# Kernel tuning notes

Hardware: AMD Instinct MI355X
Metric: run time of the kernel (lower is better)

The kernel has to match this reference:

```python
import jax, jax.numpy as jnp
import numpy as np

B, D, H, NSTEPS = 4096, 512, 2048, 16


def setup_inputs() -> dict:
    key = jax.random.key(0)
    k1, k2, k3, k4 = jax.random.split(key, 4)
    s_x = 1.0 / np.sqrt(D)
    s_h = 1.0 / np.sqrt(H)
    return {
        "z_in": jax.random.normal(k1, (B, D), dtype=jnp.float32),
        "Wx": jax.random.normal(k2, (D, H), dtype=jnp.float32) * s_x,
        "Wh": jax.random.normal(k3, (H, H), dtype=jnp.float32) * s_h,
        "bh": jnp.zeros((H,), dtype=jnp.float32),
        "Wout": jax.random.normal(k4, (H, D), dtype=jnp.float32) * s_h,
        "bout": jnp.zeros((D,), dtype=jnp.float32),
        "n_steps": NSTEPS,
    }


def reference(z_in, Wx, Wh, bh, Wout, bout, n_steps):
    # Input projection is identical every step (same z_in fed each iteration).
    xproj = z_in @ Wx + bh  # [B, H]
    h0 = jnp.zeros((z_in.shape[0], Wh.shape[0]), dtype=z_in.dtype)

    def step(h, _):
        h_new = jnp.tanh(xproj + h @ Wh)          # Elman RNN cell, hidden retained
        out = h_new @ Wout + bout                  # MLP head hidden -> latent
        return h_new, out

    _, outs = jax.lax.scan(step, h0, None, length=n_steps)  # [n_steps, B, D]
    return jnp.transpose(outs, (1, 0, 2))  # torch.stack(outs, 1) -> [B, n_steps, D]
```

## Files before the change

kernel.cpp:

```cpp
#include <hip/hip_runtime.h>
#include <hip/hip_bf16.h>
#include <stdint.h>

#define B_ 4096
#define D_ 512
#define H_ 2048
#define NS_ 16

typedef __bf16 bf16x8 __attribute__((ext_vector_type(8)));
typedef float f32x4 __attribute__((ext_vector_type(4)));
typedef short short4v __attribute__((ext_vector_type(4)));
typedef __attribute__((address_space(3))) const bf16x8* lds_frag_p;

__device__ __forceinline__ short f2bf(float f) {
  union { float f; uint32_t u; } c; c.f = f;
  uint32_t u = c.u;
  return (short)((u + 0x7fffu + ((u >> 16) & 1u)) >> 16);
}

__device__ __forceinline__ float tanh_fast(float x) {
  float e = __expf(2.0f * x);
  return 1.0f - 2.0f / (e + 1.0f);
}

__device__ __forceinline__ void gload16(const void* g, void* l) {
  __builtin_amdgcn_global_load_lds((const __attribute__((address_space(1))) void*)g,
                                   (__attribute__((address_space(3))) void*)l,
                                   16, 0, 0);
}

__global__ __launch_bounds__(256, 3) void gemm128_fusedB(
    const short* __restrict__ A, const short* __restrict__ Wfrag, int K,
    const float* __restrict__ xproj, const float* __restrict__ bias,
    float* __restrict__ outf, short* __restrict__ outh, int tout)
{
  __shared__ short lds[4 * 4096];
  const int tid = threadIdx.x, lane = tid & 63, wid = tid >> 6;
  const int wm = wid >> 1, wn = wid & 1;
  const int NT = K >> 5;

  const int g = ((int)blockIdx.x & 7) * 80 + ((int)blockIdx.x >> 3);
  const int tm = g & 31, tn = g >> 5;
  const int row0 = tm * 128, col0 = tn * 128;

  const int r0 = wid * 16 + (lane >> 2), r1 = r0 + 64;
  const int sl = lane & 3;
  const short* gA0 = A + (size_t)(row0 + r0) * K + ((sl ^ ((r0 >> 1) & 3)) << 3);
  const short* gA1 = A + (size_t)(row0 + r1) * K + ((sl ^ ((r1 >> 1) & 3)) << 3);
  const int dls = r0 * 32 + sl * 8;

  auto stageA = [&](int kt) {
    const int d = (kt & 3) * 4096 + dls;
    const size_t ko = (size_t)kt * 32;
    gload16(gA0 + ko, &lds[d]);
    gload16(gA1 + ko, &lds[d + 2048]);
  };

  const int rr = lane & 15, s4 = lane >> 4;
  int offA[4];
#pragma unroll
  for (int m = 0; m < 4; ++m) {
    int r = wm * 64 + m * 16 + rr;
    offA[m] = r * 32 + ((s4 ^ ((r >> 1) & 3)) << 3);
  }

  const short* bf = Wfrag + (size_t)(tn * 8 + wn * 4) * NT * 512 + lane * 8;

  f32x4 acc[4][4];
#pragma unroll
  for (int m = 0; m < 4; ++m)
#pragma unroll
    for (int n = 0; n < 4; ++n)
      acc[m][n] = (f32x4){0.f, 0.f, 0.f, 0.f};

  bf16x8 aX[4], bX[4], aY[4], bY[4];

  stageA(0); stageA(1); stageA(2);
#pragma unroll
  for (int n = 0; n < 4; ++n) bX[n] = *(const bf16x8*)(bf + (size_t)n * NT * 512);
  asm volatile("s_waitcnt vmcnt(0)" ::: "memory");
  __builtin_amdgcn_s_barrier();
#pragma unroll
  for (int m = 0; m < 4; ++m) aX[m] = *(lds_frag_p)&lds[offA[m]];

  auto iter = [&](int kt, bf16x8 (&ac)[4], bf16x8 (&bc)[4],
                  bf16x8 (&an)[4], bf16x8 (&bn)[4]) {
    const int kn = kt + 1;
    if (kn < NT) {
#pragma unroll
      for (int n = 0; n < 4; ++n)
        bn[n] = *(const bf16x8*)(bf + ((size_t)n * NT + kn) * 512);
    }
    if (kt + 3 < NT) stageA(kt + 3);
    if (kn < NT) {
      const int bb = (kn & 3) * 4096;
#pragma unroll
      for (int m = 0; m < 4; ++m) an[m] = *(lds_frag_p)&lds[bb + offA[m]];
    }
#pragma unroll
    for (int m = 0; m < 4; ++m)
#pragma unroll
      for (int n = 0; n < 4; ++n)
        acc[m][n] = __builtin_amdgcn_mfma_f32_16x16x32_bf16(ac[m], bc[n], acc[m][n], 0, 0, 0);
    if (kt + 3 < NT) {
      asm volatile("s_waitcnt vmcnt(2)" ::: "memory");
    } else {
      asm volatile("s_waitcnt vmcnt(0)" ::: "memory");
    }
    asm volatile("s_waitcnt lgkmcnt(0)" ::: "memory");
    if (kt < NT - 1) __builtin_amdgcn_s_barrier();
  };

  for (int kt = 0; kt < NT; kt += 2) {
    iter(kt,     aX, bX, aY, bY);
    iter(kt + 1, aY, bY, aX, bX);
  }

  const int rb = row0 + wm * 64 + ((lane >> 4) << 2);
  const int cb = col0 + wn * 64 + (lane & 15);
#pragma unroll
  for (int m = 0; m < 4; ++m) {
#pragma unroll
    for (int n = 0; n < 4; ++n) {
      const int col = cb + n * 16;
#pragma unroll
      for (int r = 0; r < 4; ++r) {
        const int row = rb + m * 16 + r;
        float v = acc[m][n][r];
        if (col < H_) {
          float x = xproj[(size_t)row * H_ + col];
          outh[(size_t)row * H_ + col] = f2bf(tanh_fast(x + v));
        } else {
          int oc = col - H_;
          outf[(size_t)row * (NS_ * D_) + tout * D_ + oc] = v + bias[oc];
        }
      }
    }
  }
}

__global__ void wfrag_build(const float* __restrict__ Wh, const float* __restrict__ Wout,
                            short* __restrict__ Wfrag) {
  const int k = blockIdx.y;
  const int col = blockIdx.x * 256 + threadIdx.x;
  float v = (col < H_) ? Wh[(size_t)k * H_ + col]
                       : Wout[(size_t)k * D_ + (col - H_)];
  Wfrag[((size_t)(col >> 4) * 64 + (k >> 5)) * 512 +
        ((k >> 3) & 3) * 128 + (col & 15) * 8 + (k & 7)] = f2bf(v);
}

template<int BM, int BN, int EPI>
__global__ __launch_bounds__(256, 2) void gemm_bt(
    const short* __restrict__ A, const short* __restrict__ Bt, int K,
    const float* __restrict__ xproj, const float* __restrict__ bias,
    float* __restrict__ outf, short* __restrict__ outh, int ldN, int tout)
{
  constexpr int WM = BM / 2, WN = BN / 2;
  constexpr int RM = WM / 16, RN = WN / 16;
  __shared__ short lds[2][(BM + BN) * 32];
  const int tid = threadIdx.x, lane = tid & 63, wid = tid >> 6;
  const int wm = wid >> 1, wn = wid & 1;
  const int row0 = blockIdx.y * BM, col0 = blockIdx.x * BN;
  const short* Ag = A + (size_t)row0 * K;
  const short* Bg = Bt + (size_t)col0 * K;

  f32x4 acc[RM][RN];
#pragma unroll
  for (int m = 0; m < RM; ++m)
#pragma unroll
    for (int n = 0; n < RN; ++n)
      acc[m][n] = (f32x4){0.f, 0.f, 0.f, 0.f};

  const int nt = K >> 5;

  auto stage = [&](int kt, int buf) {
    const short* ga = Ag + (kt << 5);
#pragma unroll
    for (int i = 0; i < BM * 4; i += 256) {
      int slot = i + tid;
      gload16(ga + (size_t)(slot >> 2) * K + ((slot & 3) << 3), &lds[buf][slot * 8]);
    }
    const short* gb = Bg + (kt << 5);
#pragma unroll
    for (int i = 0; i < BN * 4; i += 256) {
      int slot = i + tid;
      gload16(gb + (size_t)(slot >> 2) * K + ((slot & 3) << 3),
              &lds[buf][BM * 32 + slot * 8]);
    }
  };

  stage(0, 0);
  __syncthreads();
  int cur = 0;
  const int kq = (lane >> 4) << 3;
  const int rr = lane & 15;
  for (int kt = 0; kt < nt; ++kt) {
    if (kt + 1 < nt) stage(kt + 1, cur ^ 1);
    const short* la = &lds[cur][(wm * WM) * 32];
    const short* lb = &lds[cur][BM * 32 + (wn * WN) * 32];
    bf16x8 a[RM], b[RN];
#pragma unroll
    for (int m = 0; m < RM; ++m)
      a[m] = *(const bf16x8*)(la + (m * 16 + rr) * 32 + kq);
#pragma unroll
    for (int n = 0; n < RN; ++n)
      b[n] = *(const bf16x8*)(lb + (n * 16 + rr) * 32 + kq);
#pragma unroll
    for (int m = 0; m < RM; ++m)
#pragma unroll
      for (int n = 0; n < RN; ++n)
        acc[m][n] = __builtin_amdgcn_mfma_f32_16x16x32_bf16(a[m], b[n], acc[m][n], 0, 0, 0);
    __syncthreads();
    cur ^= 1;
  }

  const int rb = row0 + wm * WM + ((lane >> 4) << 2);
  const int cb = col0 + wn * WN + (lane & 15);
#pragma unroll
  for (int m = 0; m < RM; ++m) {
#pragma unroll
    for (int n = 0; n < RN; ++n) {
      const int col = cb + n * 16;
#pragma unroll
      for (int r = 0; r < 4; ++r) {
        const int row = rb + m * 16 + r;
        float v = acc[m][n][r];
        if (EPI == 0) {
          outf[(size_t)row * ldN + col] = v + bias[col];
        } else {
          outf[(size_t)row * (NS_ * D_) + tout * D_ + col] = v + bias[col];
        }
      }
    }
  }
}

__global__ void transpose_cvt(const float* __restrict__ in, short* __restrict__ out,
                              int R, int C) {
  __shared__ float tile[32][33];
  const int tx = threadIdx.x & 31, ty = threadIdx.x >> 5;
  const int c0 = blockIdx.x * 32, r0 = blockIdx.y * 32;
#pragma unroll
  for (int i = 0; i < 32; i += 8)
    tile[ty + i][tx] = in[(size_t)(r0 + ty + i) * C + c0 + tx];
  __syncthreads();
#pragma unroll
  for (int i = 0; i < 32; i += 8)
    out[(size_t)(c0 + ty + i) * R + r0 + tx] = f2bf(tile[tx][ty + i]);
}

__global__ void cvt_bf16_k(const float4* __restrict__ in, short4v* __restrict__ out, int n4) {
  int i = blockIdx.x * 256 + threadIdx.x;
  if (i >= n4) return;
  float4 v = in[i];
  short4v o;
  o[0] = f2bf(v.x); o[1] = f2bf(v.y); o[2] = f2bf(v.z); o[3] = f2bf(v.w);
  out[i] = o;
}

__global__ void tanh_h0_k(const float4* __restrict__ xp, short4v* __restrict__ h, int n4) {
  int i = blockIdx.x * 256 + threadIdx.x;
  if (i >= n4) return;
  float4 v = xp[i];
  short4v o;
  o[0] = f2bf(tanh_fast(v.x)); o[1] = f2bf(tanh_fast(v.y));
  o[2] = f2bf(tanh_fast(v.z)); o[3] = f2bf(tanh_fast(v.w));
  h[i] = o;
}

extern "C" void kernel_launch(void* const* d_in, const int* in_sizes, int n_in,
                              void* d_out, int out_size, void* d_ws, size_t ws_size,
                              hipStream_t stream) {
  const float* z    = (const float*)d_in[0];
  const float* Wx   = (const float*)d_in[1];
  const float* Wh   = (const float*)d_in[2];
  const float* bh   = (const float*)d_in[3];
  const float* Wout = (const float*)d_in[4];
  const float* bout = (const float*)d_in[5];
  float* out = (float*)d_out;

  short* zb    = (short*)d_ws;
  short* WxT   = zb + (size_t)B_ * D_;
  short* WoutT = WxT + (size_t)H_ * D_;
  short* Wfrag = WoutT + (size_t)D_ * H_;
  short* h0    = Wfrag + (size_t)(H_ + D_) * H_;
  short* h1    = h0 + (size_t)B_ * H_;
  float* xproj = (float*)(h1 + (size_t)B_ * H_);

  cvt_bf16_k<<<(B_ * D_ / 4 + 255) / 256, 256, 0, stream>>>((const float4*)z, (short4v*)zb, B_ * D_ / 4);
  transpose_cvt<<<dim3(H_ / 32, D_ / 32), 256, 0, stream>>>(Wx, WxT, D_, H_);
  transpose_cvt<<<dim3(D_ / 32, H_ / 32), 256, 0, stream>>>(Wout, WoutT, H_, D_);
  wfrag_build<<<dim3((H_ + D_) / 256, H_), 256, 0, stream>>>(Wh, Wout, Wfrag);

  gemm_bt<128, 128, 0><<<dim3(H_ / 128, B_ / 128), 256, 0, stream>>>(
      zb, WxT, D_, nullptr, bh, xproj, nullptr, H_, 0);
  tanh_h0_k<<<(B_ * H_ / 4 + 255) / 256, 256, 0, stream>>>((const float4*)xproj, (short4v*)h0, B_ * H_ / 4);

  short* hb[2] = {h0, h1};
  for (int t = 1; t <= 15; ++t) {
    const short* hp = hb[(t - 1) & 1];
    short* hn = hb[t & 1];
    gemm128_fusedB<<<640, 256, 0, stream>>>(
        hp, Wfrag, H_, xproj, bout, out, hn, t - 1);
  }
  gemm_bt<128, 64, 2><<<dim3(D_ / 64, B_ / 128), 256, 0, stream>>>(
      hb[1], WoutT, H_, nullptr, bout, out, nullptr, 0, 15);
}
```

Baseline: 1.261 ms.

## Replace LDS-staged 128x128 fused GEMM with single-wave 64x64 direct-load kernel

The recurrent step GEMM switches from a 4-wave 128x128 tile that staged A through a multi-buffered LDS ring to a single-wave 64x64 tile that loads A fragments straight from global memory into registers. This removes the LDS traffic, async-copy waits and block barriers, and gives more, smaller blocks. In exchange, A is reused less per byte loaded and the direct fragment loads are strided across rows, which increases global/L2 traffic. The epilogue branch is also hoisted to a per-block check.

```diff
diff --git a/kernel.cpp b/kernel.cpp
--- a/kernel.cpp
+++ b/kernel.cpp
@@ -10,7 +10,6 @@
 typedef __bf16 bf16x8 __attribute__((ext_vector_type(8)));
 typedef float f32x4 __attribute__((ext_vector_type(4)));
 typedef short short4v __attribute__((ext_vector_type(4)));
-typedef __attribute__((address_space(3))) const bf16x8* lds_frag_p;
 
 __device__ __forceinline__ short f2bf(float f) {
   union { float f; uint32_t u; } c; c.f = f;
@@ -29,42 +28,24 @@
                                    16, 0, 0);
 }
 
-__global__ __launch_bounds__(256, 3) void gemm128_fusedB(
+__global__ __launch_bounds__(64, 3) void gemm64_fused(
     const short* __restrict__ A, const short* __restrict__ Wfrag, int K,
     const float* __restrict__ xproj, const float* __restrict__ bias,
     float* __restrict__ outf, short* __restrict__ outh, int tout)
 {
-  __shared__ short lds[4 * 4096];
-  const int tid = threadIdx.x, lane = tid & 63, wid = tid >> 6;
-  const int wm = wid >> 1, wn = wid & 1;
+  const int lane = threadIdx.x;
+  const int rr = lane & 15, s4 = lane >> 4;
   const int NT = K >> 5;
 
-  const int g = ((int)blockIdx.x & 7) * 80 + ((int)blockIdx.x >> 3);
-  const int tm = g & 31, tn = g >> 5;
-  const int row0 = tm * 128, col0 = tn * 128;
-
-  const int r0 = wid * 16 + (lane >> 2), r1 = r0 + 64;
-  const int sl = lane & 3;
-  const short* gA0 = A + (size_t)(row0 + r0) * K + ((sl ^ ((r0 >> 1) & 3)) << 3);
-  const short* gA1 = A + (size_t)(row0 + r1) * K + ((sl ^ ((r1 >> 1) & 3)) << 3);
-  const int dls = r0 * 32 + sl * 8;
-
-  auto stageA = [&](int kt) {
-    const int d = (kt & 3) * 4096 + dls;
-    const size_t ko = (size_t)kt * 32;
-    gload16(gA0 + ko, &lds[d]);
-    gload16(gA1 + ko, &lds[d + 2048]);
-  };
-
-  const int rr = lane & 15, s4 = lane >> 4;
-  int offA[4];
-#pragma unroll
-  for (int m = 0; m < 4; ++m) {
-    int r = wm * 64 + m * 16 + rr;
-    offA[m] = r * 32 + ((s4 ^ ((r >> 1) & 3)) << 3);
-  }
-
-  const short* bf = Wfrag + (size_t)(tn * 8 + wn * 4) * NT * 512 + lane * 8;
+  const int g = ((int)blockIdx.x & 7) * 320 + ((int)blockIdx.x >> 3);
+  const int tm = g & 63, tn = g >> 6;
+  const int row0 = tm * 64, col0 = tn * 64;
+
+  const short* ga0 = A + (size_t)(row0 + 0 * 16 + rr) * K + s4 * 8;
+  const short* ga1 = A + (size_t)(row0 + 1 * 16 + rr) * K + s4 * 8;
+  const short* ga2 = A + (size_t)(row0 + 2 * 16 + rr) * K + s4 * 8;
+  const short* ga3 = A + (size_t)(row0 + 3 * 16 + rr) * K + s4 * 8;
+  const short* gb = Wfrag + (size_t)(tn * 4) * NT * 512 + lane * 8;
 
   f32x4 acc[4][4];
 #pragma unroll
@@ -75,40 +56,31 @@
 
   bf16x8 aX[4], bX[4], aY[4], bY[4];
 
-  stageA(0); stageA(1); stageA(2);
-#pragma unroll
-  for (int n = 0; n < 4; ++n) bX[n] = *(const bf16x8*)(bf + (size_t)n * NT * 512);
-  asm volatile("s_waitcnt vmcnt(0)" ::: "memory");
-  __builtin_amdgcn_s_barrier();
-#pragma unroll
-  for (int m = 0; m < 4; ++m) aX[m] = *(lds_frag_p)&lds[offA[m]];
+  aX[0] = *(const bf16x8*)(ga0);
+  aX[1] = *(const bf16x8*)(ga1);
+  aX[2] = *(const bf16x8*)(ga2);
+  aX[3] = *(const bf16x8*)(ga3);
+#pragma unroll
+  for (int n = 0; n < 4; ++n) bX[n] = *(const bf16x8*)(gb + (size_t)n * NT * 512);
 
   auto iter = [&](int kt, bf16x8 (&ac)[4], bf16x8 (&bc)[4],
                   bf16x8 (&an)[4], bf16x8 (&bn)[4]) {
     const int kn = kt + 1;
     if (kn < NT) {
+      const size_t ko = (size_t)kn * 32;
+      an[0] = *(const bf16x8*)(ga0 + ko);
+      an[1] = *(const bf16x8*)(ga1 + ko);
+      an[2] = *(const bf16x8*)(ga2 + ko);
+      an[3] = *(const bf16x8*)(ga3 + ko);
 #pragma unroll
       for (int n = 0; n < 4; ++n)
-        bn[n] = *(const bf16x8*)(bf + ((size_t)n * NT + kn) * 512);
-    }
-    if (kt + 3 < NT) stageA(kt + 3);
-    if (kn < NT) {
-      const int bb = (kn & 3) * 4096;
-#pragma unroll
-      for (int m = 0; m < 4; ++m) an[m] = *(lds_frag_p)&lds[bb + offA[m]];
+        bn[n] = *(const bf16x8*)(gb + ((size_t)n * NT + kn) * 512);
     }
 #pragma unroll
     for (int m = 0; m < 4; ++m)
 #pragma unroll
       for (int n = 0; n < 4; ++n)
         acc[m][n] = __builtin_amdgcn_mfma_f32_16x16x32_bf16(ac[m], bc[n], acc[m][n], 0, 0, 0);
-    if (kt + 3 < NT) {
-      asm volatile("s_waitcnt vmcnt(2)" ::: "memory");
-    } else {
-      asm volatile("s_waitcnt vmcnt(0)" ::: "memory");
-    }
-    asm volatile("s_waitcnt lgkmcnt(0)" ::: "memory");
-    if (kt < NT - 1) __builtin_amdgcn_s_barrier();
   };
 
   for (int kt = 0; kt < NT; kt += 2) {
@@ -116,23 +88,32 @@
     iter(kt + 1, aY, bY, aX, bX);
   }
 
-  const int rb = row0 + wm * 64 + ((lane >> 4) << 2);
-  const int cb = col0 + wn * 64 + (lane & 15);
-#pragma unroll
-  for (int m = 0; m < 4; ++m) {
-#pragma unroll
-    for (int n = 0; n < 4; ++n) {
-      const int col = cb + n * 16;
-#pragma unroll
-      for (int r = 0; r < 4; ++r) {
-        const int row = rb + m * 16 + r;
-        float v = acc[m][n][r];
-        if (col < H_) {
+  const int rb = row0 + s4 * 4;
+  const int cb = col0 + rr;
+  if (col0 < H_) {
+#pragma unroll
+    for (int m = 0; m < 4; ++m) {
+#pragma unroll
+      for (int n = 0; n < 4; ++n) {
+        const int col = cb + n * 16;
+#pragma unroll
+        for (int r = 0; r < 4; ++r) {
+          const int row = rb + m * 16 + r;
           float x = xproj[(size_t)row * H_ + col];
-          outh[(size_t)row * H_ + col] = f2bf(tanh_fast(x + v));
-        } else {
-          int oc = col - H_;
-          outf[(size_t)row * (NS_ * D_) + tout * D_ + oc] = v + bias[oc];
+          outh[(size_t)row * H_ + col] = f2bf(tanh_fast(x + acc[m][n][r]));
+        }
+      }
+    }
+  } else {
+#pragma unroll
+    for (int m = 0; m < 4; ++m) {
+#pragma unroll
+      for (int n = 0; n < 4; ++n) {
+        const int oc = cb - H_ + n * 16;
+#pragma unroll
+        for (int r = 0; r < 4; ++r) {
+          const int row = rb + m * 16 + r;
+          outf[(size_t)row * (NS_ * D_) + tout * D_ + oc] = acc[m][n][r] + bias[oc];
         }
       }
     }
@@ -300,7 +281,7 @@
   for (int t = 1; t <= 15; ++t) {
     const short* hp = hb[(t - 1) & 1];
     short* hn = hb[t & 1];
-    gemm128_fusedB<<<640, 256, 0, stream>>>(
+    gemm64_fused<<<2560, 64, 0, stream>>>(
         hp, Wfrag, H_, xproj, bout, out, hn, t - 1);
   }
   gemm_bt<128, 64, 2><<<dim3(D_ / 64, B_ / 128), 256, 0, stream>>>(
```

Result: slower. 1.660 ms (+31.7%).
